# Optimization experiments

Hardware: AMD Instinct MI355X
Metric: run time of the kernel (lower is better)

Reference implementation:

```python
import jax, jax.numpy as jnp
import numpy as np

N_NODES = 10000
N_EDGES = 320000
CH = 64          # multiplicity per irrep (64x0e node feats)
R_DIM = 8        # radial embedding dim
L_MAX = 2
N_L = L_MAX + 1
SH_DIM = 9       # 1 + 3 + 5
AVG_NEIGH = 32.0
MLP_HID = 64


def setup_inputs() -> dict:
    key = jax.random.key(0)
    ks = jax.random.split(key, 11)
    return {
        "edge_vectors": jax.random.normal(ks[0], (N_EDGES, 3), jnp.float32),
        "node_feats": jax.random.normal(ks[1], (N_NODES, CH), jnp.float32),
        "radial_embeddings": jax.random.normal(ks[2], (N_EDGES, R_DIM), jnp.float32),
        "senders": jax.random.randint(ks[3], (N_EDGES,), 0, N_NODES),
        "receivers": jax.random.randint(ks[4], (N_EDGES,), 0, N_NODES),
        # learned params (e3nn Linear / MLP weights, unit normal init)
        "W_up": jax.random.normal(ks[5], (CH, CH), jnp.float32),
        "W_mlp1": jax.random.normal(ks[6], (R_DIM, MLP_HID), jnp.float32),
        "W_mlp2": jax.random.normal(ks[7], (MLP_HID, MLP_HID), jnp.float32),
        "W_mlp3": jax.random.normal(ks[8], (MLP_HID, MLP_HID), jnp.float32),
        "W_mlp4": jax.random.normal(ks[9], (MLP_HID, N_L * CH), jnp.float32),
        "W_down": jax.random.normal(ks[10], (N_L, CH, CH), jnp.float32),
    }


def spherical_harmonics(vec):
    """Component-normalized real spherical harmonics (||Y_l||^2 = 2l+1), l=0..2,
    on normalized edge vectors (e3nn normalize=True, normalization='component')."""
    v = vec / jnp.linalg.norm(vec, axis=-1, keepdims=True)
    x, y, z = v[..., 0], v[..., 1], v[..., 2]
    c15 = float(np.sqrt(15.0))
    c5 = float(np.sqrt(5.0))
    sh2 = jnp.stack(
        [c15 * x * y, c15 * y * z, 0.5 * c5 * (3.0 * z * z - 1.0),
         c15 * x * z, 0.5 * c15 * (x * x - y * y)], axis=-1)
    return jnp.concatenate(
        [jnp.ones_like(x)[..., None], float(np.sqrt(3.0)) * v, sh2], axis=-1)  # [E, 9]


def reference(edge_vectors, node_feats, radial_embeddings, senders, receivers,
              W_up, W_mlp1, W_mlp2, W_mlp3, W_mlp4, W_down):
    inv_ch = 1.0 / np.sqrt(CH)
    n_nodes = node_feats.shape[0]

    # linear_up: scalar irreps -> plain channel mixing with e3nn 1/sqrt(fan_in)
    h = (node_feats @ W_up) * inv_ch                               # [N, CH]

    sh = spherical_harmonics(edge_vectors)                         # [E, 9]

    # radial MLP -> one weight per (channel, l) tensor-product path
    m = radial_embeddings
    for W in (W_mlp1, W_mlp2, W_mlp3):
        m = jax.nn.silu((m @ W) / np.sqrt(W.shape[0]))
    mix = (m @ W_mlp4) / np.sqrt(MLP_HID)                          # [E, N_L*CH]
    w = mix.reshape(-1, N_L, CH).transpose(0, 2, 1)                # [E, CH, N_L]
    # broadcast each per-irrep weight over its 2l+1 components
    w = jnp.repeat(w, np.array([1, 3, 5]), axis=-1,
                   total_repeat_length=SH_DIM)                     # [E, CH, 9]

    # tensor product (scalar node feats x Y_l) with radial weights: messages
    msg = h[senders][:, :, None] * sh[:, None, :] * w              # [E, CH, 9]

    # scatter-add to receivers, normalize by avg_num_neighbors
    agg = jax.ops.segment_sum(msg.reshape(msg.shape[0], -1),
                              receivers, num_segments=n_nodes)
    agg = (agg / AVG_NEIGH).reshape(n_nodes, CH, SH_DIM)           # [N, CH, 9]

    # linear_down: independent channel mixing per l (equivariant Linear)
    outs = []
    start = 0
    for l in range(N_L):
        d = 2 * l + 1
        o = jnp.einsum('ncm,cd->ndm', agg[:, :, start:start + d], W_down[l]) * inv_ch
        outs.append(o.reshape(n_nodes, -1))
        start += d
    return jnp.concatenate(outs, axis=-1)                          # [N, 576]
```

## Files before the change

kernel.cpp:

```cpp
#include <hip/hip_runtime.h>
#include <hip/hip_bf16.h>
#include <math.h>

#define N_NODES 10000
#define N_EDGES 320000
#define CH 64
#define MIXW 192
#define EREC 12

#define W1_OFF 0
#define W2_OFF 512
#define W3_OFF 5120
#define W4_OFF 9728
#define W_TOT 23552
#define ACT_STRIDE 72

#define EPB 128

#define PREP_BLKS 92
#define H_BLKS 2500
#define HIST_BLKS 1250

typedef __attribute__((ext_vector_type(8))) short bf16x8;
typedef __attribute__((ext_vector_type(4))) float f32x4;
#define MFMA16(a, b, c) __builtin_amdgcn_mfma_f32_16x16x32_bf16(a, b, c, 0, 0, 0)

__device__ __forceinline__ float bf2f(unsigned short u) {
    union { unsigned int i; float f; } v; v.i = ((unsigned int)u) << 16; return v.f;
}
__device__ __forceinline__ unsigned short f2bf(float f) {
    __hip_bfloat16 b = __float2bfloat16(f);
    return *reinterpret_cast<unsigned short*>(&b);
}
__device__ __forceinline__ float silu(float t) {
    return t * __builtin_amdgcn_rcpf(1.0f + __expf(-t));
}

__global__ __launch_bounds__(256) void k_pre(const float* __restrict__ W1,
                                             const float* __restrict__ W2,
                                             const float* __restrict__ W3,
                                             const float* __restrict__ W4,
                                             unsigned short* __restrict__ wimg,
                                             const float* __restrict__ nf,
                                             const float* __restrict__ Wup,
                                             float* __restrict__ h,
                                             const int* __restrict__ recv,
                                             int* __restrict__ counts) {
    int bid = blockIdx.x;
    int t = threadIdx.x;
    if (bid < PREP_BLKS) {
        int i = bid * 256 + t;
        if (i >= W_TOT) return;
        float v;
        if (i < W2_OFF) {
            int n = i >> 3, k = i & 7;
            v = W1[k * 64 + n];
        } else if (i < W3_OFF) {
            int j = i - W2_OFF; int n = j / 72, k = j % 72;
            v = (k < 64) ? W2[k * 64 + n] * 0.125f : 0.f;
        } else if (i < W4_OFF) {
            int j = i - W3_OFF; int n = j / 72, k = j % 72;
            v = (k < 64) ? W3[k * 64 + n] * 0.125f : 0.f;
        } else {
            int j = i - W4_OFF; int n = j / 72, k = j % 72;
            v = (k < 64) ? W4[k * MIXW + n] : 0.f;
        }
        wimg[i] = f2bf(v);
    } else if (bid < PREP_BLKS + H_BLKS) {
        int node = __builtin_amdgcn_readfirstlane((bid - PREP_BLKS) * 4 + (t >> 6));
        int lane = t & 63;
        const float* nrow = nf + (size_t)node * CH;
        float acc = 0.f;
#pragma unroll
        for (int k = 0; k < CH; ++k) acc += nrow[k] * Wup[k * CH + lane];
        h[(size_t)node * CH + lane] = acc * 0.015625f;
    } else {
        int e = (bid - PREP_BLKS - H_BLKS) * 256 + t;
        atomicAdd(&counts[recv[e]], 1);
    }
}

__global__ __launch_bounds__(1024) void k_scan(const int* __restrict__ counts,
                                               int* __restrict__ offsets,
                                               int* __restrict__ cursor) {
    __shared__ int part[1024];
    int t = threadIdx.x;
    const int CHUNK = 10;
    int base = t * CHUNK;
    int s = 0;
    for (int i = 0; i < CHUNK; ++i) {
        int idx = base + i;
        if (idx < N_NODES) s += counts[idx];
    }
    part[t] = s;
    __syncthreads();
    for (int off = 1; off < 1024; off <<= 1) {
        int v = 0;
        if (t >= off) v = part[t - off];
        __syncthreads();
        part[t] += v;
        __syncthreads();
    }
    int run = part[t] - s;
    for (int i = 0; i < CHUNK; ++i) {
        int idx = base + i;
        if (idx < N_NODES) {
            offsets[idx] = run;
            cursor[idx] = run;
            run += counts[idx];
        }
    }
    if (t == 1023) offsets[N_NODES] = part[1023];
}

__global__ __launch_bounds__(256) void k_mlp(const float* __restrict__ ev,
                                             const float* __restrict__ rad,
                                             const unsigned short* __restrict__ wimg,
                                             const int* __restrict__ senders,
                                             const int* __restrict__ recv,
                                             int* __restrict__ cursor,
                                             const float* __restrict__ h,
                                             unsigned short* __restrict__ hw,
                                             float* __restrict__ erec) {
    __shared__ unsigned short act[EPB * ACT_STRIDE];
    __shared__ int s_pos[EPB];
    __shared__ int s_snd[EPB];

    const int t = threadIdx.x;
    const int e0 = blockIdx.x * EPB;
    const int wv = t >> 6;
    const int lane = t & 63;
    const int lrow = lane & 15;
    const int quad = lane >> 4;
    const int wr0 = wv * 32;
    const int em0 = wr0 + lrow;
    const int em1 = em0 + 16;
    const int cr0 = wr0 + quad * 4;
    const int cr1 = cr0 + 16;

    if (lane < 32) {
        int e = e0 + wr0 + lane;
        int p = atomicAdd(&cursor[recv[e]], 1);
        s_pos[wr0 + lane] = p;
        s_snd[wr0 + lane] = senders[e];
        float vx = ev[(size_t)e * 3 + 0], vy = ev[(size_t)e * 3 + 1], vz = ev[(size_t)e * 3 + 2];
        float inv = rsqrtf(vx * vx + vy * vy + vz * vz);
        float x = vx * inv, y = vy * inv, z = vz * inv;
        const float s3 = 1.7320508075688772f;
        const float s15 = 3.872983346207417f;
        const float s5 = 2.2360679774997896f;
        float4* rp = (float4*)(erec + (size_t)p * EREC);
        rp[0] = make_float4(1.0f, s3 * x, s3 * y, s3 * z);
        rp[1] = make_float4(s15 * x * y, s15 * y * z, 0.5f * s5 * (3.0f * z * z - 1.0f), s15 * x * z);
        rp[2] = make_float4(0.5f * s15 * (x * x - y * y), 0.f, 0.f, 0.f);
    }

    bf16x8 ar0 = {0, 0, 0, 0, 0, 0, 0, 0};
    bf16x8 ar1 = {0, 0, 0, 0, 0, 0, 0, 0};
    if (quad == 0) {
        const float4* rp0 = (const float4*)(rad + (size_t)(e0 + em0) * 8);
        const float4* rp1 = (const float4*)(rad + (size_t)(e0 + em1) * 8);
        float4 u = rp0[0], v = rp0[1];
        ar0[0] = (short)f2bf(u.x); ar0[1] = (short)f2bf(u.y);
        ar0[2] = (short)f2bf(u.z); ar0[3] = (short)f2bf(u.w);
        ar0[4] = (short)f2bf(v.x); ar0[5] = (short)f2bf(v.y);
        ar0[6] = (short)f2bf(v.z); ar0[7] = (short)f2bf(v.w);
        u = rp1[0]; v = rp1[1];
        ar1[0] = (short)f2bf(u.x); ar1[1] = (short)f2bf(u.y);
        ar1[2] = (short)f2bf(u.z); ar1[3] = (short)f2bf(u.w);
        ar1[4] = (short)f2bf(v.x); ar1[5] = (short)f2bf(v.y);
        ar1[6] = (short)f2bf(v.z); ar1[7] = (short)f2bf(v.w);
    }

#pragma unroll
    for (int nt = 0; nt < 4; ++nt) {
        bf16x8 bw = {0, 0, 0, 0, 0, 0, 0, 0};
        if (quad == 0) bw = *(const bf16x8*)(wimg + W1_OFF + (nt * 16 + lrow) * 8);
        f32x4 c0 = {0.f, 0.f, 0.f, 0.f};
        f32x4 c1 = {0.f, 0.f, 0.f, 0.f};
        c0 = MFMA16(ar0, bw, c0);
        c1 = MFMA16(ar1, bw, c1);
#pragma unroll
        for (int r = 0; r < 4; ++r) {
            act[(cr0 + r) * ACT_STRIDE + nt * 16 + lrow] =
                f2bf(silu(c0[r] * 0.3535533905932738f));
            act[(cr1 + r) * ACT_STRIDE + nt * 16 + lrow] =
                f2bf(silu(c1[r] * 0.3535533905932738f));
        }
    }

#pragma unroll
    for (int L = 0; L < 2; ++L) {
        const unsigned short* wbase = wimg + (L == 0 ? W2_OFF : W3_OFF);
        bf16x8 a00 = *(const bf16x8*)(act + em0 * ACT_STRIDE + quad * 8);
        bf16x8 a01 = *(const bf16x8*)(act + em0 * ACT_STRIDE + 32 + quad * 8);
        bf16x8 a10 = *(const bf16x8*)(act + em1 * ACT_STRIDE + quad * 8);
        bf16x8 a11 = *(const bf16x8*)(act + em1 * ACT_STRIDE + 32 + quad * 8);
        bf16x8 b[4][2];
#pragma unroll
        for (int nt = 0; nt < 4; ++nt)
#pragma unroll
            for (int kh = 0; kh < 2; ++kh)
                b[nt][kh] = *(const bf16x8*)(wbase + (nt * 16 + lrow) * 72 + kh * 32 + quad * 8);
#pragma unroll
        for (int nt = 0; nt < 4; ++nt) {
            f32x4 c0 = {0.f, 0.f, 0.f, 0.f};
            f32x4 c1 = {0.f, 0.f, 0.f, 0.f};
            c0 = MFMA16(a00, b[nt][0], c0);
            c0 = MFMA16(a01, b[nt][1], c0);
            c1 = MFMA16(a10, b[nt][0], c1);
            c1 = MFMA16(a11, b[nt][1], c1);
#pragma unroll
            for (int r = 0; r < 4; ++r) {
                act[(cr0 + r) * ACT_STRIDE + nt * 16 + lrow] = f2bf(silu(c0[r]));
                act[(cr1 + r) * ACT_STRIDE + nt * 16 + lrow] = f2bf(silu(c1[r]));
            }
        }
    }

    {
        bf16x8 a00 = *(const bf16x8*)(act + em0 * ACT_STRIDE + quad * 8);
        bf16x8 a01 = *(const bf16x8*)(act + em0 * ACT_STRIDE + 32 + quad * 8);
        bf16x8 a10 = *(const bf16x8*)(act + em1 * ACT_STRIDE + quad * 8);
        bf16x8 a11 = *(const bf16x8*)(act + em1 * ACT_STRIDE + 32 + quad * 8);

        float hreg0[4][4], hreg1[4][4];
#pragma unroll
        for (int r = 0; r < 4; ++r) {
            int sn0 = s_snd[cr0 + r];
            int sn1 = s_snd[cr1 + r];
            const float* hb0 = h + (size_t)sn0 * CH + lrow;
            const float* hb1 = h + (size_t)sn1 * CH + lrow;
#pragma unroll
            for (int ntl = 0; ntl < 4; ++ntl) {
                hreg0[r][ntl] = hb0[ntl * 16];
                hreg1[r][ntl] = hb1[ntl * 16];
            }
        }

#pragma unroll
        for (int T = 0; T < 3; ++T) {
            bf16x8 b[4][2];
#pragma unroll
            for (int ntl = 0; ntl < 4; ++ntl)
#pragma unroll
                for (int kh = 0; kh < 2; ++kh)
                    b[ntl][kh] = *(const bf16x8*)(wimg + W4_OFF +
                        ((T * 4 + ntl) * 16 + lrow) * 72 + kh * 32 + quad * 8);
#pragma unroll
            for (int ntl = 0; ntl < 4; ++ntl) {
                f32x4 c0 = {0.f, 0.f, 0.f, 0.f};
                f32x4 c1 = {0.f, 0.f, 0.f, 0.f};
                c0 = MFMA16(a00, b[ntl][0], c0);
                c0 = MFMA16(a01, b[ntl][1], c0);
                c1 = MFMA16(a10, b[ntl][0], c1);
                c1 = MFMA16(a11, b[ntl][1], c1);
#pragma unroll
                for (int r = 0; r < 4; ++r) {
                    act[(cr0 + r) * ACT_STRIDE + ntl * 16 + lrow] =
                        f2bf(c0[r] * hreg0[r][ntl]);
                    act[(cr1 + r) * ACT_STRIDE + ntl * 16 + lrow] =
                        f2bf(c1[r] * hreg1[r][ntl]);
                }
            }
#pragma unroll
            for (int j = 0; j < 4; ++j) {
                int idx = lane + 64 * j;
                int row = idx >> 3, c8 = idx & 7;
                int p = s_pos[wr0 + row];
                uint4 v = *(const uint4*)(act + (wr0 + row) * ACT_STRIDE + c8 * 8);
                *(uint4*)(hw + (size_t)p * MIXW + T * 64 + c8 * 8) = v;
            }
        }
    }
}

__global__ __launch_bounds__(256, 4) void k_aggdown(const int* __restrict__ offsets,
                                                    const float* __restrict__ erec,
                                                    const unsigned short* __restrict__ hw,
                                                    const float* __restrict__ Wd,
                                                    float* __restrict__ out) {
    __shared__ float sg[4][576];
    int wv = threadIdx.x >> 6;
    int lane = threadIdx.x & 63;
    int node = __builtin_amdgcn_readfirstlane(blockIdx.x * 4 + wv);
    int s0 = __builtin_amdgcn_readfirstlane(offsets[node]);
    int s1 = __builtin_amdgcn_readfirstlane(offsets[node + 1]);
    float acc[9] = {0.f, 0.f, 0.f, 0.f, 0.f, 0.f, 0.f, 0.f, 0.f};
#pragma unroll 4
    for (int i = s0; i < s1; ++i) {
        const float* rp = erec + (size_t)i * EREC;
        const unsigned short* hrow = hw + (size_t)i * MIXW;
        float w0 = bf2f(hrow[lane]);
        float w1 = bf2f(hrow[64 + lane]);
        float w2 = bf2f(hrow[128 + lane]);
        acc[0] += w0 * rp[0];
        acc[1] += w1 * rp[1];
        acc[2] += w1 * rp[2];
        acc[3] += w1 * rp[3];
        acc[4] += w2 * rp[4];
        acc[5] += w2 * rp[5];
        acc[6] += w2 * rp[6];
        acc[7] += w2 * rp[7];
        acc[8] += w2 * rp[8];
    }
    float* arow = sg[wv];
#pragma unroll
    for (int m = 0; m < 9; ++m) arow[lane * 9 + m] = acc[m] * (1.0f / 32.0f);

    float* orow = out + (size_t)node * 576;
    {
        float a = 0.f;
#pragma unroll
        for (int c = 0; c < 64; ++c) a += arow[c * 9] * Wd[c * 64 + lane];
        orow[lane] = a * 0.125f;
    }
    {
        float m3[3] = {0.f, 0.f, 0.f};
#pragma unroll
        for (int c = 0; c < 64; ++c) {
            float w = Wd[(64 + c) * 64 + lane];
#pragma unroll
            for (int mm = 0; mm < 3; ++mm) m3[mm] += arow[c * 9 + 1 + mm] * w;
        }
#pragma unroll
        for (int mm = 0; mm < 3; ++mm) orow[64 + lane * 3 + mm] = m3[mm] * 0.125f;
    }
    {
        float m5[5] = {0.f, 0.f, 0.f, 0.f, 0.f};
#pragma unroll
        for (int c = 0; c < 64; ++c) {
            float w = Wd[(128 + c) * 64 + lane];
#pragma unroll
            for (int mm = 0; mm < 5; ++mm) m5[mm] += arow[c * 9 + 4 + mm] * w;
        }
#pragma unroll
        for (int mm = 0; mm < 5; ++mm) orow[256 + lane * 5 + mm] = m5[mm] * 0.125f;
    }
}

static inline size_t align256(size_t x) { return (x + 255) & ~(size_t)255; }

extern "C" void kernel_launch(void* const* d_in, const int* in_sizes, int n_in,
                              void* d_out, int out_size, void* d_ws, size_t ws_size,
                              hipStream_t stream) {
    const float* edge_vectors = (const float*)d_in[0];
    const float* node_feats   = (const float*)d_in[1];
    const float* radial       = (const float*)d_in[2];
    const int*   senders      = (const int*)d_in[3];
    const int*   receivers    = (const int*)d_in[4];
    const float* W_up         = (const float*)d_in[5];
    const float* W_mlp1       = (const float*)d_in[6];
    const float* W_mlp2       = (const float*)d_in[7];
    const float* W_mlp3       = (const float*)d_in[8];
    const float* W_mlp4       = (const float*)d_in[9];
    const float* W_down       = (const float*)d_in[10];
    float* out = (float*)d_out;

    char* base = (char*)d_ws;
    size_t off = 0;
    float* h = (float*)(base + off);              off = align256(off + (size_t)N_NODES * CH * 4);
    unsigned short* hw = (unsigned short*)(base + off); off = align256(off + (size_t)N_EDGES * MIXW * 2);
    float* erec = (float*)(base + off);           off = align256(off + (size_t)N_EDGES * EREC * 4);
    unsigned short* wimg = (unsigned short*)(base + off); off = align256(off + (size_t)W_TOT * 2);
    int* counts = (int*)(base + off);             off = align256(off + (size_t)N_NODES * 4);
    int* offsets = (int*)(base + off);            off = align256(off + (size_t)(N_NODES + 1) * 4);
    int* cursor = (int*)(base + off);             off = align256(off + (size_t)N_NODES * 4);

    hipMemsetAsync(counts, 0, (size_t)N_NODES * 4, stream);

    k_pre<<<PREP_BLKS + H_BLKS + HIST_BLKS, 256, 0, stream>>>(
        W_mlp1, W_mlp2, W_mlp3, W_mlp4, wimg, node_feats, W_up, h, receivers, counts);
    k_scan<<<1, 1024, 0, stream>>>(counts, offsets, cursor);
    k_mlp<<<N_EDGES / EPB, 256, 0, stream>>>(edge_vectors, radial, wimg, senders,
                                             receivers, cursor, h, hw, erec);
    k_aggdown<<<N_NODES / 4, 256, 0, stream>>>(offsets, erec, hw, W_down, out);
}
```

Baseline: 218.6 us.

## Prefetch MLP weight fragments, batch h rows, warp-shuffle scan, deeper agg unroll

Restructures the per-edge MLP kernel to double-buffer weight fragments in registers, loading the next layer's B fragments before computing the current layer. It also moves the sender-feature gather ahead of the last layer so those loads are in flight earlier. The W1 scale is folded into the prepacked weights. The h projection now computes four nodes per wave so each Wup value is reused four times, and the scan replaces the LDS Hillis-Steele loop with wave shuffles. The aggregation loop is unrolled deeper. The extra live fragment registers may raise register pressure and reduce occupancy in the MLP kernel.

```diff
diff --git a/kernel.cpp b/kernel.cpp
--- a/kernel.cpp
+++ b/kernel.cpp
@@ -18,7 +18,7 @@
 #define EPB 128
 
 #define PREP_BLKS 92
-#define H_BLKS 2500
+#define H_BLKS 625
 #define HIST_BLKS 1250
 
 typedef __attribute__((ext_vector_type(8))) short bf16x8;
@@ -34,6 +34,72 @@
 }
 __device__ __forceinline__ float silu(float t) {
     return t * __builtin_amdgcn_rcpf(1.0f + __expf(-t));
+}
+
+__device__ __forceinline__ void load_bfrag(bf16x8 (&b)[4][2],
+                                           const unsigned short* __restrict__ wbase,
+                                           int lrow, int quad) {
+#pragma unroll
+    for (int nt = 0; nt < 4; ++nt)
+#pragma unroll
+        for (int kh = 0; kh < 2; ++kh)
+            b[nt][kh] = *(const bf16x8*)(wbase + (nt * 16 + lrow) * 72 + kh * 32 + quad * 8);
+}
+
+__device__ __forceinline__ void layer64(unsigned short* act, const bf16x8 (&b)[4][2],
+                                        int em0, int em1, int cr0, int cr1,
+                                        int lrow, int quad) {
+    bf16x8 a00 = *(const bf16x8*)(act + em0 * ACT_STRIDE + quad * 8);
+    bf16x8 a01 = *(const bf16x8*)(act + em0 * ACT_STRIDE + 32 + quad * 8);
+    bf16x8 a10 = *(const bf16x8*)(act + em1 * ACT_STRIDE + quad * 8);
+    bf16x8 a11 = *(const bf16x8*)(act + em1 * ACT_STRIDE + 32 + quad * 8);
+#pragma unroll
+    for (int nt = 0; nt < 4; ++nt) {
+        f32x4 c0 = {0.f, 0.f, 0.f, 0.f};
+        f32x4 c1 = {0.f, 0.f, 0.f, 0.f};
+        c0 = MFMA16(a00, b[nt][0], c0);
+        c0 = MFMA16(a01, b[nt][1], c0);
+        c1 = MFMA16(a10, b[nt][0], c1);
+        c1 = MFMA16(a11, b[nt][1], c1);
+#pragma unroll
+        for (int r = 0; r < 4; ++r) {
+            act[(cr0 + r) * ACT_STRIDE + nt * 16 + lrow] = f2bf(silu(c0[r]));
+            act[(cr1 + r) * ACT_STRIDE + nt * 16 + lrow] = f2bf(silu(c1[r]));
+        }
+    }
+}
+
+__device__ __forceinline__ void l4_third(unsigned short* act,
+                                         const int (&pj)[4],
+                                         unsigned short* __restrict__ hw,
+                                         const bf16x8 (&b)[4][2],
+                                         const bf16x8& a00, const bf16x8& a01,
+                                         const bf16x8& a10, const bf16x8& a11,
+                                         const float (&hreg0)[4][4],
+                                         const float (&hreg1)[4][4],
+                                         int T, int cr0, int cr1, int wr0,
+                                         int lane, int lrow, int quad) {
+#pragma unroll
+    for (int ntl = 0; ntl < 4; ++ntl) {
+        f32x4 c0 = {0.f, 0.f, 0.f, 0.f};
+        f32x4 c1 = {0.f, 0.f, 0.f, 0.f};
+        c0 = MFMA16(a00, b[ntl][0], c0);
+        c0 = MFMA16(a01, b[ntl][1], c0);
+        c1 = MFMA16(a10, b[ntl][0], c1);
+        c1 = MFMA16(a11, b[ntl][1], c1);
+#pragma unroll
+        for (int r = 0; r < 4; ++r) {
+            act[(cr0 + r) * ACT_STRIDE + ntl * 16 + lrow] = f2bf(c0[r] * hreg0[r][ntl]);
+            act[(cr1 + r) * ACT_STRIDE + ntl * 16 + lrow] = f2bf(c1[r] * hreg1[r][ntl]);
+        }
+    }
+#pragma unroll
+    for (int j = 0; j < 4; ++j) {
+        int idx = lane + 64 * j;
+        int row = idx >> 3, c8 = idx & 7;
+        uint4 v = *(const uint4*)(act + (wr0 + row) * ACT_STRIDE + c8 * 8);
+        *(uint4*)(hw + (size_t)pj[j] * MIXW + T * 64 + c8 * 8) = v;
+    }
 }
 
 __global__ __launch_bounds__(256) void k_pre(const float* __restrict__ W1,
@@ -54,7 +120,7 @@
         float v;
         if (i < W2_OFF) {
             int n = i >> 3, k = i & 7;
-            v = W1[k * 64 + n];
+            v = W1[k * 64 + n] * 0.35355339059327376f;
         } else if (i < W3_OFF) {
             int j = i - W2_OFF; int n = j / 72, k = j % 72;
             v = (k < 64) ? W2[k * 64 + n] * 0.125f : 0.f;
@@ -67,13 +133,23 @@
         }
         wimg[i] = f2bf(v);
     } else if (bid < PREP_BLKS + H_BLKS) {
-        int node = __builtin_amdgcn_readfirstlane((bid - PREP_BLKS) * 4 + (t >> 6));
+        int nb = __builtin_amdgcn_readfirstlane(
+            (bid - PREP_BLKS) * 16 + (t >> 6) * 4);
         int lane = t & 63;
-        const float* nrow = nf + (size_t)node * CH;
-        float acc = 0.f;
-#pragma unroll
-        for (int k = 0; k < CH; ++k) acc += nrow[k] * Wup[k * CH + lane];
-        h[(size_t)node * CH + lane] = acc * 0.015625f;
+        const float* nrow = nf + (size_t)nb * CH;
+        float a0 = 0.f, a1 = 0.f, a2 = 0.f, a3 = 0.f;
+#pragma unroll
+        for (int k = 0; k < CH; ++k) {
+            float w = Wup[k * CH + lane];
+            a0 = fmaf(nrow[k], w, a0);
+            a1 = fmaf(nrow[CH + k], w, a1);
+            a2 = fmaf(nrow[2 * CH + k], w, a2);
+            a3 = fmaf(nrow[3 * CH + k], w, a3);
+        }
+        h[(size_t)nb * CH + lane] = a0 * 0.015625f;
+        h[(size_t)(nb + 1) * CH + lane] = a1 * 0.015625f;
+        h[(size_t)(nb + 2) * CH + lane] = a2 * 0.015625f;
+        h[(size_t)(nb + 3) * CH + lane] = a3 * 0.015625f;
     } else {
         int e = (bid - PREP_BLKS - H_BLKS) * 256 + t;
         atomicAdd(&counts[recv[e]], 1);
@@ -83,7 +159,7 @@
 __global__ __launch_bounds__(1024) void k_scan(const int* __restrict__ counts,
                                                int* __restrict__ offsets,
                                                int* __restrict__ cursor) {
-    __shared__ int part[1024];
+    __shared__ int wsum[16];
     int t = threadIdx.x;
     const int CHUNK = 10;
     int base = t * CHUNK;
@@ -92,16 +168,27 @@
         int idx = base + i;
         if (idx < N_NODES) s += counts[idx];
     }
-    part[t] = s;
+    int lane = t & 63, wv = t >> 6;
+    int x = s;
+#pragma unroll
+    for (int off = 1; off < 64; off <<= 1) {
+        int y = __shfl_up(x, off, 64);
+        if (lane >= off) x += y;
+    }
+    if (lane == 63) wsum[wv] = x;
     __syncthreads();
-    for (int off = 1; off < 1024; off <<= 1) {
-        int v = 0;
-        if (t >= off) v = part[t - off];
-        __syncthreads();
-        part[t] += v;
-        __syncthreads();
-    }
-    int run = part[t] - s;
+    if (wv == 0 && lane < 16) {
+        int v = wsum[lane];
+#pragma unroll
+        for (int off = 1; off < 16; off <<= 1) {
+            int y = __shfl_up(v, off, 64);
+            if (lane >= off) v += y;
+        }
+        wsum[lane] = v;
+    }
+    __syncthreads();
+    int wbase = (wv == 0) ? 0 : wsum[wv - 1];
+    int run = wbase + x - s;
     for (int i = 0; i < CHUNK; ++i) {
         int idx = base + i;
         if (idx < N_NODES) {
@@ -110,7 +197,7 @@
             run += counts[idx];
         }
     }
-    if (t == 1023) offsets[N_NODES] = part[1023];
+    if (t == 1023) offsets[N_NODES] = wbase + x;
 }
 
 __global__ __launch_bounds__(256) void k_mlp(const float* __restrict__ ev,
@@ -137,6 +224,31 @@
     const int em1 = em0 + 16;
     const int cr0 = wr0 + quad * 4;
     const int cr1 = cr0 + 16;
+
+    bf16x8 ar0 = {0, 0, 0, 0, 0, 0, 0, 0};
+    bf16x8 ar1 = {0, 0, 0, 0, 0, 0, 0, 0};
+    bf16x8 bw1[4];
+#pragma unroll
+    for (int nt = 0; nt < 4; ++nt) bw1[nt] = (bf16x8){0, 0, 0, 0, 0, 0, 0, 0};
+    if (quad == 0) {
+        const float4* rp0 = (const float4*)(rad + (size_t)(e0 + em0) * 8);
+        const float4* rp1 = (const float4*)(rad + (size_t)(e0 + em1) * 8);
+        float4 u = rp0[0], v = rp0[1];
+        ar0[0] = (short)f2bf(u.x); ar0[1] = (short)f2bf(u.y);
+        ar0[2] = (short)f2bf(u.z); ar0[3] = (short)f2bf(u.w);
+        ar0[4] = (short)f2bf(v.x); ar0[5] = (short)f2bf(v.y);
+        ar0[6] = (short)f2bf(v.z); ar0[7] = (short)f2bf(v.w);
+        u = rp1[0]; v = rp1[1];
+        ar1[0] = (short)f2bf(u.x); ar1[1] = (short)f2bf(u.y);
+        ar1[2] = (short)f2bf(u.z); ar1[3] = (short)f2bf(u.w);
+        ar1[4] = (short)f2bf(v.x); ar1[5] = (short)f2bf(v.y);
+        ar1[6] = (short)f2bf(v.z); ar1[7] = (short)f2bf(v.w);
+#pragma unroll
+        for (int nt = 0; nt < 4; ++nt)
+            bw1[nt] = *(const bf16x8*)(wimg + W1_OFF + (nt * 16 + lrow) * 8);
+    }
+    bf16x8 bA[4][2], bB[4][2];
+    load_bfrag(bA, wimg + W2_OFF, lrow, quad);
 
     if (lane < 32) {
         int e = e0 + wr0 + lane;
@@ -155,66 +267,40 @@
         rp[2] = make_float4(0.5f * s15 * (x * x - y * y), 0.f, 0.f, 0.f);
     }
 
-    bf16x8 ar0 = {0, 0, 0, 0, 0, 0, 0, 0};
-    bf16x8 ar1 = {0, 0, 0, 0, 0, 0, 0, 0};
-    if (quad == 0) {
-        const float4* rp0 = (const float4*)(rad + (size_t)(e0 + em0) * 8);
-        const float4* rp1 = (const float4*)(rad + (size_t)(e0 + em1) * 8);
-        float4 u = rp0[0], v = rp0[1];
-        ar0[0] = (short)f2bf(u.x); ar0[1] = (short)f2bf(u.y);
-        ar0[2] = (short)f2bf(u.z); ar0[3] = (short)f2bf(u.w);
-        ar0[4] = (short)f2bf(v.x); ar0[5] = (short)f2bf(v.y);
-        ar0[6] = (short)f2bf(v.z); ar0[7] = (short)f2bf(v.w);
-        u = rp1[0]; v = rp1[1];
-        ar1[0] = (short)f2bf(u.x); ar1[1] = (short)f2bf(u.y);
-        ar1[2] = (short)f2bf(u.z); ar1[3] = (short)f2bf(u.w);
-        ar1[4] = (short)f2bf(v.x); ar1[5] = (short)f2bf(v.y);
-        ar1[6] = (short)f2bf(v.z); ar1[7] = (short)f2bf(v.w);
-    }
-
 #pragma unroll
     for (int nt = 0; nt < 4; ++nt) {
-        bf16x8 bw = {0, 0, 0, 0, 0, 0, 0, 0};
-        if (quad == 0) bw = *(const bf16x8*)(wimg + W1_OFF + (nt * 16 + lrow) * 8);
         f32x4 c0 = {0.f, 0.f, 0.f, 0.f};
         f32x4 c1 = {0.f, 0.f, 0.f, 0.f};
-        c0 = MFMA16(ar0, bw, c0);
-        c1 = MFMA16(ar1, bw, c1);
+        c0 = MFMA16(ar0, bw1[nt], c0);
+        c1 = MFMA16(ar1, bw1[nt], c1);
 #pragma unroll
         for (int r = 0; r < 4; ++r) {
-            act[(cr0 + r) * ACT_STRIDE + nt * 16 + lrow] =
-                f2bf(silu(c0[r] * 0.3535533905932738f));
-            act[(cr1 + r) * ACT_STRIDE + nt * 16 + lrow] =
-                f2bf(silu(c1[r] * 0.3535533905932738f));
-        }
-    }
-
-#pragma unroll
-    for (int L = 0; L < 2; ++L) {
-        const unsigned short* wbase = wimg + (L == 0 ? W2_OFF : W3_OFF);
-        bf16x8 a00 = *(const bf16x8*)(act + em0 * ACT_STRIDE + quad * 8);
-        bf16x8 a01 = *(const bf16x8*)(act + em0 * ACT_STRIDE + 32 + quad * 8);
-        bf16x8 a10 = *(const bf16x8*)(act + em1 * ACT_STRIDE + quad * 8);
-        bf16x8 a11 = *(const bf16x8*)(act + em1 * ACT_STRIDE + 32 + quad * 8);
-        bf16x8 b[4][2];
-#pragma unroll
-        for (int nt = 0; nt < 4; ++nt)
-#pragma unroll
-            for (int kh = 0; kh < 2; ++kh)
-                b[nt][kh] = *(const bf16x8*)(wbase + (nt * 16 + lrow) * 72 + kh * 32 + quad * 8);
-#pragma unroll
-        for (int nt = 0; nt < 4; ++nt) {
-            f32x4 c0 = {0.f, 0.f, 0.f, 0.f};
-            f32x4 c1 = {0.f, 0.f, 0.f, 0.f};
-            c0 = MFMA16(a00, b[nt][0], c0);
-            c0 = MFMA16(a01, b[nt][1], c0);
-            c1 = MFMA16(a10, b[nt][0], c1);
-            c1 = MFMA16(a11, b[nt][1], c1);
-#pragma unroll
-            for (int r = 0; r < 4; ++r) {
-                act[(cr0 + r) * ACT_STRIDE + nt * 16 + lrow] = f2bf(silu(c0[r]));
-                act[(cr1 + r) * ACT_STRIDE + nt * 16 + lrow] = f2bf(silu(c1[r]));
-            }
+            act[(cr0 + r) * ACT_STRIDE + nt * 16 + lrow] = f2bf(silu(c0[r]));
+            act[(cr1 + r) * ACT_STRIDE + nt * 16 + lrow] = f2bf(silu(c1[r]));
+        }
+    }
+
+    load_bfrag(bB, wimg + W3_OFF, lrow, quad);
+    layer64(act, bA, em0, em1, cr0, cr1, lrow, quad);
+
+    load_bfrag(bA, wimg + W4_OFF, lrow, quad);
+    int sn0[4], sn1[4];
+#pragma unroll
+    for (int r = 0; r < 4; ++r) {
+        sn0[r] = s_snd[cr0 + r];
+        sn1[r] = s_snd[cr1 + r];
+    }
+    layer64(act, bB, em0, em1, cr0, cr1, lrow, quad);
+
+    float hreg0[4][4], hreg1[4][4];
+#pragma unroll
+    for (int r = 0; r < 4; ++r) {
+        const float* hb0 = h + (size_t)sn0[r] * CH + lrow;
+        const float* hb1 = h + (size_t)sn1[r] * CH + lrow;
+#pragma unroll
+        for (int ntl = 0; ntl < 4; ++ntl) {
+            hreg0[r][ntl] = hb0[ntl * 16];
+            hreg1[r][ntl] = hb1[ntl * 16];
         }
     }
 
@@ -223,55 +309,18 @@
         bf16x8 a01 = *(const bf16x8*)(act + em0 * ACT_STRIDE + 32 + quad * 8);
         bf16x8 a10 = *(const bf16x8*)(act + em1 * ACT_STRIDE + quad * 8);
         bf16x8 a11 = *(const bf16x8*)(act + em1 * ACT_STRIDE + 32 + quad * 8);
-
-        float hreg0[4][4], hreg1[4][4];
-#pragma unroll
-        for (int r = 0; r < 4; ++r) {
-            int sn0 = s_snd[cr0 + r];
-            int sn1 = s_snd[cr1 + r];
-            const float* hb0 = h + (size_t)sn0 * CH + lrow;
-            const float* hb1 = h + (size_t)sn1 * CH + lrow;
-#pragma unroll
-            for (int ntl = 0; ntl < 4; ++ntl) {
-                hreg0[r][ntl] = hb0[ntl * 16];
-                hreg1[r][ntl] = hb1[ntl * 16];
-            }
-        }
-
-#pragma unroll
-        for (int T = 0; T < 3; ++T) {
-            bf16x8 b[4][2];
-#pragma unroll
-            for (int ntl = 0; ntl < 4; ++ntl)
-#pragma unroll
-                for (int kh = 0; kh < 2; ++kh)
-                    b[ntl][kh] = *(const bf16x8*)(wimg + W4_OFF +
-                        ((T * 4 + ntl) * 16 + lrow) * 72 + kh * 32 + quad * 8);
-#pragma unroll
-            for (int ntl = 0; ntl < 4; ++ntl) {
-                f32x4 c0 = {0.f, 0.f, 0.f, 0.f};
-                f32x4 c1 = {0.f, 0.f, 0.f, 0.f};
-                c0 = MFMA16(a00, b[ntl][0], c0);
-                c0 = MFMA16(a01, b[ntl][1], c0);
-                c1 = MFMA16(a10, b[ntl][0], c1);
-                c1 = MFMA16(a11, b[ntl][1], c1);
-#pragma unroll
-                for (int r = 0; r < 4; ++r) {
-                    act[(cr0 + r) * ACT_STRIDE + ntl * 16 + lrow] =
-                        f2bf(c0[r] * hreg0[r][ntl]);
-                    act[(cr1 + r) * ACT_STRIDE + ntl * 16 + lrow] =
-                        f2bf(c1[r] * hreg1[r][ntl]);
-                }
-            }
-#pragma unroll
-            for (int j = 0; j < 4; ++j) {
-                int idx = lane + 64 * j;
-                int row = idx >> 3, c8 = idx & 7;
-                int p = s_pos[wr0 + row];
-                uint4 v = *(const uint4*)(act + (wr0 + row) * ACT_STRIDE + c8 * 8);
-                *(uint4*)(hw + (size_t)p * MIXW + T * 64 + c8 * 8) = v;
-            }
-        }
+        int pj[4];
+#pragma unroll
+        for (int j = 0; j < 4; ++j) pj[j] = s_pos[wr0 + ((lane + 64 * j) >> 3)];
+
+        load_bfrag(bB, wimg + W4_OFF + 64 * 72, lrow, quad);
+        l4_third(act, pj, hw, bA, a00, a01, a10, a11, hreg0, hreg1,
+                 0, cr0, cr1, wr0, lane, lrow, quad);
+        load_bfrag(bA, wimg + W4_OFF + 2 * 64 * 72, lrow, quad);
+        l4_third(act, pj, hw, bB, a00, a01, a10, a11, hreg0, hreg1,
+                 1, cr0, cr1, wr0, lane, lrow, quad);
+        l4_third(act, pj, hw, bA, a00, a01, a10, a11, hreg0, hreg1,
+                 2, cr0, cr1, wr0, lane, lrow, quad);
     }
 }
 
@@ -287,7 +336,7 @@
     int s0 = __builtin_amdgcn_readfirstlane(offsets[node]);
     int s1 = __builtin_amdgcn_readfirstlane(offsets[node + 1]);
     float acc[9] = {0.f, 0.f, 0.f, 0.f, 0.f, 0.f, 0.f, 0.f, 0.f};
-#pragma unroll 4
+#pragma unroll 8
     for (int i = s0; i < s1; ++i) {
         const float* rp = erec + (size_t)i * EREC;
         const unsigned short* hrow = hw + (size_t)i * MIXW;
```

New measurement: 206.6 us. 1.06x faster.
